# Kernel optimization log

Hardware: AMD Instinct MI355X
Metric: run time of the kernel (lower is better)

## Reference

```python
import jax, jax.numpy as jnp
import numpy as np


def _simple_rnn(x_tbd, Wx, Wh, b, return_sequences):
    # x_tbd: [T, B, D]; h_t = tanh(x_t @ Wx + h_{t-1} @ Wh + b)
    B = x_tbd.shape[1]
    H = Wh.shape[0]
    # precompute input projection for all steps (single big GEMM)
    xw = jnp.einsum('tbd,dh->tbh', x_tbd, Wx) + b

    def step(h, xw_t):
        h_new = jnp.tanh(xw_t + h @ Wh)
        return h_new, h_new if return_sequences else None

    h0 = jnp.zeros((B, H), dtype=x_tbd.dtype)
    h_last, hs = jax.lax.scan(step, h0, xw)
    return hs if return_sequences else h_last


def setup_inputs() -> dict:
    key = jax.random.key(0)
    ks = jax.random.split(key, 8)
    B, T, D, H, C = 32, 1024, 128, 512, 10
    s_in = 1.0 / np.sqrt(D)
    s_h = 1.0 / np.sqrt(H)
    return {
        'x': jax.random.normal(ks[0], (B, T, D), jnp.float32),
        'Wx1': jax.random.normal(ks[1], (D, H), jnp.float32) * s_in,
        'Wh1': jax.random.normal(ks[2], (H, H), jnp.float32) * s_h,
        'b1': jnp.zeros((H,), jnp.float32),
        'Wx2': jax.random.normal(ks[3], (H, H), jnp.float32) * s_h,
        'Wh2': jax.random.normal(ks[4], (H, H), jnp.float32) * s_h,
        'b2': jnp.zeros((H,), jnp.float32),
        'Wo': jax.random.normal(ks[5], (H, C), jnp.float32) * s_h,
        'bo': jnp.zeros((C,), jnp.float32),
    }


def reference(x, Wx1, Wh1, b1, Wx2, Wh2, b2, Wo, bo):
    # x: [B, T, D] -> time-major [T, B, D]
    x_t = jnp.swapaxes(x, 0, 1)
    h1 = _simple_rnn(x_t, Wx1, Wh1, b1, return_sequences=True)   # [T, B, H]
    h2 = _simple_rnn(h1, Wx2, Wh2, b2, return_sequences=False)   # [B, H]
    logits = h2 @ Wo + bo
    return jax.nn.softmax(logits, axis=-1)
```

## Files before the change

### kernel.cpp

```cpp
#include <hip/hip_runtime.h>
#include <hip/hip_fp16.h>
#include <math.h>

#define BATCH 32
#define TLEN  1024
#define DIN   128
#define HID   512
#define NCLS  10
#define NB    2
#define NGRP  (BATCH/NB)
#define NSL   8
#define RING  32
#define SENTV 0xFFFFFFFFu
#define SENT64 0xFFFFFFFFFFFFFFFFull
#define POLL_CAP (1u<<17)

typedef _Float16 hf2 __attribute__((ext_vector_type(2)));

__device__ __forceinline__ unsigned aload(const unsigned* p) {
  return __hip_atomic_load(p, __ATOMIC_RELAXED, __HIP_MEMORY_SCOPE_AGENT);
}
__device__ __forceinline__ void astore(unsigned* p, unsigned v) {
  __hip_atomic_store(p, v, __ATOMIC_RELAXED, __HIP_MEMORY_SCOPE_AGENT);
}
__device__ __forceinline__ unsigned long long aload64(const unsigned long long* p) {
  return __hip_atomic_load(p, __ATOMIC_RELAXED, __HIP_MEMORY_SCOPE_AGENT);
}
__device__ __forceinline__ void astore64(unsigned long long* p, unsigned long long v) {
  __hip_atomic_store(p, v, __ATOMIC_RELAXED, __HIP_MEMORY_SCOPE_AGENT);
}
__device__ __forceinline__ int aloadi(const int* p) {
  return __hip_atomic_load(p, __ATOMIC_RELAXED, __HIP_MEMORY_SCOPE_AGENT);
}
__device__ __forceinline__ void astorei(int* p, int v) {
  __hip_atomic_store(p, v, __ATOMIC_RELAXED, __HIP_MEMORY_SCOPE_AGENT);
}

__device__ __forceinline__ float fdot2u(unsigned a, unsigned b, float c) {
#if __has_builtin(__builtin_amdgcn_fdot2)
  return __builtin_amdgcn_fdot2(__builtin_bit_cast(hf2, a),
                                __builtin_bit_cast(hf2, b), c, false);
#else
  hf2 av = __builtin_bit_cast(hf2, a), bv = __builtin_bit_cast(hf2, b);
  return c + (float)av[0] * (float)bv[0] + (float)av[1] * (float)bv[1];
#endif
}

__device__ __forceinline__ unsigned packh2(float lo, float hi) {
  __half2 h = __floats2half2_rn(lo, hi);
  return __builtin_bit_cast(unsigned, h);
}

__global__ __launch_bounds__(256) void k_xw1(
    const float* __restrict__ x, const float* __restrict__ Wx1,
    const float* __restrict__ b1, unsigned* __restrict__ xw1)
{
  __shared__ float xst[DIN * 4];
  const int tid  = threadIdx.x;
  const int row0 = blockIdx.x * 4;
  for (int idx = tid; idx < 4 * DIN; idx += 256) {
    int r = idx >> 7, d = idx & (DIN - 1);
    int row = row0 + r;
    int t = row >> 5, b = row & 31;
    xst[d * 4 + r] = x[((size_t)b * TLEN + t) * DIN + d];
  }
  __syncthreads();
  float acc[4][2];
#pragma unroll
  for (int r = 0; r < 4; ++r) { acc[r][0] = 0.f; acc[r][1] = 0.f; }
  const int j0 = 2 * tid, j1 = 2 * tid + 1;
  for (int d = 0; d < DIN; ++d) {
    float w0 = Wx1[(size_t)d * HID + j0];
    float w1 = Wx1[(size_t)d * HID + j1];
    float4 xv = *reinterpret_cast<const float4*>(&xst[d * 4]);
    acc[0][0] += xv.x * w0; acc[0][1] += xv.x * w1;
    acc[1][0] += xv.y * w0; acc[1][1] += xv.y * w1;
    acc[2][0] += xv.z * w0; acc[2][1] += xv.z * w1;
    acc[3][0] += xv.w * w0; acc[3][1] += xv.w * w1;
  }
  float bb0 = b1[j0], bb1 = b1[j1];
#pragma unroll
  for (int r = 0; r < 4; ++r)
    xw1[(size_t)(row0 + r) * 256 + tid] = packh2(acc[r][0] + bb0, acc[r][1] + bb1);
}

__global__ __launch_bounds__(512) void k_rnn(
    const unsigned* __restrict__ xw1,
    const float* __restrict__ Wh1,
    const float* __restrict__ Wx2, const float* __restrict__ Wh2,
    const float* __restrict__ b2,
    unsigned* __restrict__ ring1,
    unsigned* __restrict__ ringC,
    int* __restrict__ prog2,
    float* __restrict__ h2fin)
{
  const int tid  = threadIdx.x;
  const int wgid = blockIdx.x;
  const int xcd   = wgid & 7;
  const int mm    = wgid >> 3;
  const int sl    = mm & 7;
  const int layer = (mm >> 3) & 1;
  const int g     = ((mm >> 4) << 3) | xcd;
  const int b0 = g * NB;
  const int c0 = sl * 64;
  const int w  = tid >> 6, l = tid & 63;
  const int q  = l >> 4;
  const int lo = l & 15;
  const int o  = w * 16 + lo;
  const int obb = o >> 6, oj = o & 63;
  const int ocol = c0 + oj;

  const int pu = tid & 127;

  __shared__ __align__(16) unsigned h_s[2][NB][512];

  if (layer == 0) {
    const int pb = (tid >> 7) & 1;
    unsigned wreg[64];
    {
      const int k0 = q * 128;
#pragma unroll
      for (int i = 0; i < 16; ++i) {
        const int rr = 4 * ((i + q) & 15);
#pragma unroll
        for (int j = 0; j < 4; ++j) {
          const int k = k0 + 2 * (rr + j);
          wreg[4 * i + j] = packh2(Wh1[(size_t)k * HID + ocol],
                                   Wh1[(size_t)(k + 1) * HID + ocol]);
        }
      }
    }
    int cached = -1;
    for (int t = 0; t < TLEN; ++t) {
      const int p = t & 1;
      unsigned long long v64 = 0;
      const unsigned long long* pp = nullptr;
      if (tid < 256 && t > 0) {
        pp = (const unsigned long long*)
             &ring1[((size_t)((t - 1) & (RING - 1)) * BATCH + b0 + pb) * 256 + 2 * pu];
        v64 = aload64(pp);
      }
      unsigned xww = 0;
      if (q == 0)
        xww = xw1[((size_t)t * BATCH + b0 + obb) * 256 + (ocol >> 1)];
      if (w == 0) {
        const int need = t - (RING - 6);
        if (cached < need) {
          unsigned it = 0;
          for (;;) {
            int pr = (l < NSL) ? aloadi(&prog2[g * NSL + l]) : 0x7fffffff;
#pragma unroll
            for (int d = 1; d < NSL; d <<= 1) pr = min(pr, __shfl_xor(pr, d));
            pr = __shfl(pr, 0);
            cached = pr;
            if (cached >= need || ++it >= POLL_CAP) break;
          }
        }
        if (l < 32) {
          int rb = l >> 4, jj = l & 15;
          astore64((unsigned long long*)
                   &ring1[((size_t)((t + 1) & (RING - 1)) * BATCH + b0 + rb) * 256
                          + (c0 >> 1) + 2 * jj], SENT64);
        }
      }
      if (tid < 256) {
        if (t > 0) {
          unsigned v0 = (unsigned)v64, v1 = (unsigned)(v64 >> 32);
          if (v0 == SENTV || v1 == SENTV) {
            unsigned it = 0;
            do {
              unsigned long long nv = aload64(pp);
              v0 = (unsigned)nv; v1 = (unsigned)(nv >> 32);
            } while ((v0 == SENTV || v1 == SENTV) && ++it < POLL_CAP);
            if (v0 == SENTV) v0 = 0;
            if (v1 == SENTV) v1 = 0;
            v64 = ((unsigned long long)v1 << 32) | v0;
          }
        }
        *(unsigned long long*)&h_s[p][pb][2 * pu] = v64;
      }
      __syncthreads();
      float acc = 0.f;
      const unsigned* hp = &h_s[p][obb][q * 64];
#pragma unroll
      for (int i = 0; i < 16; ++i) {
        const int rr = 4 * ((i + q) & 15);
        uint4 hv = *reinterpret_cast<const uint4*>(&hp[rr]);
        acc = fdot2u(hv.x, wreg[4 * i + 0], acc);
        acc = fdot2u(hv.y, wreg[4 * i + 1], acc);
        acc = fdot2u(hv.z, wreg[4 * i + 2], acc);
        acc = fdot2u(hv.w, wreg[4 * i + 3], acc);
      }
      acc += __shfl_xor(acc, 16);
      acc += __shfl_xor(acc, 32);
      if (q == 0) {
        hf2 xv = __builtin_bit_cast(hf2, xww);
        float z = (float)xv[oj & 1] + acc;
        float h = tanhf(z);
        float hn = __shfl_down(h, 1);
        if (!(lo & 1))
          astore(&ring1[((size_t)(t & (RING - 1)) * BATCH + b0 + obb) * 256 + (ocol >> 1)],
                 packh2(h, hn));
      }
    }
  } else {
    const int set = tid >> 7;
    unsigned wreg[128];
    {
      const int k0 = q * 256;
#pragma unroll
      for (int i = 0; i < 32; ++i) {
        const int rr = 4 * ((i + q) & 31);
#pragma unroll
        for (int j = 0; j < 4; ++j) {
          const int k = k0 + 2 * (rr + j);
          float a, b;
          if (k < HID) {
            a = Wx2[(size_t)k * HID + ocol];
            b = Wx2[(size_t)(k + 1) * HID + ocol];
          } else {
            a = Wh2[(size_t)(k - HID) * HID + ocol];
            b = Wh2[(size_t)(k - HID + 1) * HID + ocol];
          }
          wreg[4 * i + j] = packh2(a, b);
        }
      }
    }
    float b2v = (q == 0) ? b2[ocol] : 0.f;
    for (int t = 0; t < TLEN; ++t) {
      const int p = t & 1;
      unsigned long long v64 = 0;
      const unsigned long long* pp = nullptr;
      if (set < 2) {
        pp = (const unsigned long long*)
             &ring1[((size_t)(t & (RING - 1)) * BATCH + b0 + set) * 256 + 2 * pu];
        v64 = aload64(pp);
      } else if (t > 0) {
        pp = (const unsigned long long*)
             &ringC[((size_t)((t - 1) & (RING - 1)) * BATCH + b0 + (set - 2)) * 256 + 2 * pu];
        v64 = aload64(pp);
      }
      if (w == 0 && l < 32) {
        int rb = l >> 4, jj = l & 15;
        astore64((unsigned long long*)
                 &ringC[((size_t)((t + 1) & (RING - 1)) * BATCH + b0 + rb) * 256
                        + (c0 >> 1) + 2 * jj], SENT64);
      }
      if (pp) {
        unsigned v0 = (unsigned)v64, v1 = (unsigned)(v64 >> 32);
        if (v0 == SENTV || v1 == SENTV) {
          unsigned it = 0;
          do {
            unsigned long long nv = aload64(pp);
            v0 = (unsigned)nv; v1 = (unsigned)(nv >> 32);
          } while ((v0 == SENTV || v1 == SENTV) && ++it < POLL_CAP);
          if (v0 == SENTV) v0 = 0;
          if (v1 == SENTV) v1 = 0;
          v64 = ((unsigned long long)v1 << 32) | v0;
        }
      }
      {
        const int bb = set & 1;
        const int base = (set >> 1) * 256;
        *(unsigned long long*)&h_s[p][bb][base + 2 * pu] = v64;
      }
      __syncthreads();
      if (tid == 0) astorei(&prog2[g * NSL + sl], t);
      float acc = 0.f;
      const unsigned* hp = &h_s[p][obb][q * 128];
#pragma unroll
      for (int i = 0; i < 32; ++i) {
        const int rr = 4 * ((i + q) & 31);
        uint4 hv = *reinterpret_cast<const uint4*>(&hp[rr]);
        acc = fdot2u(hv.x, wreg[4 * i + 0], acc);
        acc = fdot2u(hv.y, wreg[4 * i + 1], acc);
        acc = fdot2u(hv.z, wreg[4 * i + 2], acc);
        acc = fdot2u(hv.w, wreg[4 * i + 3], acc);
      }
      acc += __shfl_xor(acc, 16);
      acc += __shfl_xor(acc, 32);
      if (q == 0) {
        float z = b2v + acc;
        float h = tanhf(z);
        if (t == TLEN - 1) h2fin[(size_t)(b0 + obb) * HID + ocol] = h;
        float hn = __shfl_down(h, 1);
        if (!(lo & 1))
          astore(&ringC[((size_t)(t & (RING - 1)) * BATCH + b0 + obb) * 256 + (ocol >> 1)],
                 packh2(h, hn));
      }
    }
  }
}

__global__ __launch_bounds__(640) void k_head(
    const float* __restrict__ h2, const float* __restrict__ Wo,
    const float* __restrict__ bo, float* __restrict__ out)
{
  __shared__ float lg[16];
  const int b = blockIdx.x;
  const int c = threadIdx.x >> 6;
  const int l = threadIdx.x & 63;
  float p = 0.f;
#pragma unroll
  for (int i = 0; i < 8; ++i) {
    int k = l + 64 * i;
    p += h2[(size_t)b * HID + k] * Wo[(size_t)k * NCLS + c];
  }
  for (int off = 32; off; off >>= 1) p += __shfl_down(p, off);
  if (l == 0) lg[c] = p + bo[c];
  __syncthreads();
  if (threadIdx.x == 0) {
    float m = lg[0];
    for (int i = 1; i < NCLS; ++i) m = fmaxf(m, lg[i]);
    float e[NCLS];
    float s = 0.f;
    for (int i = 0; i < NCLS; ++i) { e[i] = expf(lg[i] - m); s += e[i]; }
    for (int i = 0; i < NCLS; ++i) out[(size_t)b * NCLS + i] = e[i] / s;
  }
}

extern "C" void kernel_launch(void* const* d_in, const int* in_sizes, int n_in,
                              void* d_out, int out_size, void* d_ws, size_t ws_size,
                              hipStream_t stream)
{
  (void)in_sizes; (void)n_in; (void)out_size; (void)ws_size;
  const float* x   = (const float*)d_in[0];
  const float* Wx1 = (const float*)d_in[1];
  const float* Wh1 = (const float*)d_in[2];
  const float* b1  = (const float*)d_in[3];
  const float* Wx2 = (const float*)d_in[4];
  const float* Wh2 = (const float*)d_in[5];
  const float* b2  = (const float*)d_in[6];
  const float* Wo  = (const float*)d_in[7];
  const float* bo  = (const float*)d_in[8];
  float* out = (float*)d_out;

  char* ws = (char*)d_ws;
  size_t o = 0;
  unsigned* xw1 = (unsigned*)(ws + o); o += (size_t)TLEN * BATCH * 256 * 4;
  const size_t ringBytes = (size_t)RING * BATCH * 256 * 4;
  unsigned* ring1 = (unsigned*)(ws + o); o += ringBytes;
  unsigned* ringC = (unsigned*)(ws + o); o += ringBytes;
  int* prog2 = (int*)(ws + o); o += 1024;
  float* h2fin = (float*)(ws + o); o += (size_t)BATCH * HID * 4;

  hipMemsetAsync(ring1, 0xFF, 2 * ringBytes, stream);
  hipMemsetAsync(prog2, 0xFF, NGRP * NSL * 4, stream);

  k_xw1<<<TLEN * BATCH / 4, 256, 0, stream>>>(x, Wx1, b1, xw1);
  k_rnn<<<256, 512, 0, stream>>>(xw1, Wh1, Wx2, Wh2, b2,
                                 ring1, ringC, prog2, h2fin);
  k_head<<<BATCH, 640, 0, stream>>>(h2fin, Wo, bo, out);
}
```

Baseline: 1.983 ms.

## Interleave two batch pairs per workgroup to halve RNN workgroup count

Each workgroup now owns four batch rows, processed as two interleaved pairs per timestep, so the grid drops from 256 to 128 workgroups. Each pair keeps its own shared-memory buffer, progress counter and sentinel ring handshake, so while one pair waits on its ring data the workgroup can work on the other. This cuts the number of polling workgroups and the cross-XCD traffic. The cost is twice the serial per-step work in each workgroup, plus an extra __syncthreads per step. The XCD-aware workgroup mapping is also replaced by a simpler index split.

```diff
diff --git a/kernel.cpp b/kernel.cpp
--- a/kernel.cpp
+++ b/kernel.cpp
@@ -7,8 +7,7 @@
 #define DIN   128
 #define HID   512
 #define NCLS  10
-#define NB    2
-#define NGRP  (BATCH/NB)
+#define NGR   8
 #define NSL   8
 #define RING  32
 #define SENTV 0xFFFFFFFFu
@@ -96,12 +95,10 @@
 {
   const int tid  = threadIdx.x;
   const int wgid = blockIdx.x;
-  const int xcd   = wgid & 7;
-  const int mm    = wgid >> 3;
-  const int sl    = mm & 7;
-  const int layer = (mm >> 3) & 1;
-  const int g     = ((mm >> 4) << 3) | xcd;
-  const int b0 = g * NB;
+  const int g     = wgid & 7;
+  const int sl    = (wgid >> 3) & 7;
+  const int layer = wgid >> 6;
+  const int b0 = g * 4;
   const int c0 = sl * 64;
   const int w  = tid >> 6, l = tid & 63;
   const int q  = l >> 4;
@@ -112,7 +109,7 @@
 
   const int pu = tid & 127;
 
-  __shared__ __align__(16) unsigned h_s[2][NB][512];
+  __shared__ __align__(16) unsigned h_s[2][2][2][512];
 
   if (layer == 0) {
     const int pb = (tid >> 7) & 1;
@@ -130,41 +127,130 @@
         }
       }
     }
-    int cached = -1;
+    int cached[2] = {-1, -1};
     for (int t = 0; t < TLEN; ++t) {
-      const int p = t & 1;
-      unsigned long long v64 = 0;
-      const unsigned long long* pp = nullptr;
-      if (tid < 256 && t > 0) {
-        pp = (const unsigned long long*)
-             &ring1[((size_t)((t - 1) & (RING - 1)) * BATCH + b0 + pb) * 256 + 2 * pu];
-        v64 = aload64(pp);
+      const int par = t & 1;
+#pragma unroll
+      for (int pr = 0; pr < 2; ++pr) {
+        const int bbase = b0 + 2 * pr;
+        unsigned long long v64 = 0;
+        const unsigned long long* pp = nullptr;
+        if (tid < 256 && t > 0) {
+          pp = (const unsigned long long*)
+               &ring1[((size_t)((t - 1) & (RING - 1)) * BATCH + bbase + pb) * 256 + 2 * pu];
+          v64 = aload64(pp);
+        }
+        unsigned xww = 0;
+        if (q == 0)
+          xww = xw1[((size_t)t * BATCH + bbase + obb) * 256 + (ocol >> 1)];
+        if (w == 0) {
+          const int need = t - (RING - 6);
+          if (cached[pr] < need) {
+            unsigned it = 0;
+            for (;;) {
+              int p2 = (l < NSL) ? aloadi(&prog2[((g * NSL + l) << 1) + pr]) : 0x7fffffff;
+#pragma unroll
+              for (int d = 1; d < NSL; d <<= 1) p2 = min(p2, __shfl_xor(p2, d));
+              p2 = __shfl(p2, 0);
+              cached[pr] = p2;
+              if (cached[pr] >= need || ++it >= POLL_CAP) break;
+            }
+          }
+          if (l < 32) {
+            int rb = l >> 4, jj = l & 15;
+            astore64((unsigned long long*)
+                     &ring1[((size_t)((t + 1) & (RING - 1)) * BATCH + bbase + rb) * 256
+                            + (c0 >> 1) + 2 * jj], SENT64);
+          }
+        }
+        if (tid < 256) {
+          if (t > 0) {
+            unsigned v0 = (unsigned)v64, v1 = (unsigned)(v64 >> 32);
+            if (v0 == SENTV || v1 == SENTV) {
+              unsigned it = 0;
+              do {
+                unsigned long long nv = aload64(pp);
+                v0 = (unsigned)nv; v1 = (unsigned)(nv >> 32);
+              } while ((v0 == SENTV || v1 == SENTV) && ++it < POLL_CAP);
+              if (v0 == SENTV) v0 = 0;
+              if (v1 == SENTV) v1 = 0;
+              v64 = ((unsigned long long)v1 << 32) | v0;
+            }
+          }
+          *(unsigned long long*)&h_s[pr][par][pb][2 * pu] = v64;
+        }
+        __syncthreads();
+        float acc = 0.f;
+        const unsigned* hp = &h_s[pr][par][obb][q * 64];
+#pragma unroll
+        for (int i = 0; i < 16; ++i) {
+          const int rr = 4 * ((i + q) & 15);
+          uint4 hv = *reinterpret_cast<const uint4*>(&hp[rr]);
+          acc = fdot2u(hv.x, wreg[4 * i + 0], acc);
+          acc = fdot2u(hv.y, wreg[4 * i + 1], acc);
+          acc = fdot2u(hv.z, wreg[4 * i + 2], acc);
+          acc = fdot2u(hv.w, wreg[4 * i + 3], acc);
+        }
+        acc += __shfl_xor(acc, 16);
+        acc += __shfl_xor(acc, 32);
+        if (q == 0) {
+          hf2 xv = __builtin_bit_cast(hf2, xww);
+          float z = (float)xv[oj & 1] + acc;
+          float h = tanhf(z);
+          float hn = __shfl_down(h, 1);
+          if (!(lo & 1))
+            astore(&ring1[((size_t)(t & (RING - 1)) * BATCH + bbase + obb) * 256 + (ocol >> 1)],
+                   packh2(h, hn));
+        }
       }
-      unsigned xww = 0;
-      if (q == 0)
-        xww = xw1[((size_t)t * BATCH + b0 + obb) * 256 + (ocol >> 1)];
-      if (w == 0) {
-        const int need = t - (RING - 6);
-        if (cached < need) {
-          unsigned it = 0;
-          for (;;) {
-            int pr = (l < NSL) ? aloadi(&prog2[g * NSL + l]) : 0x7fffffff;
-#pragma unroll
-            for (int d = 1; d < NSL; d <<= 1) pr = min(pr, __shfl_xor(pr, d));
-            pr = __shfl(pr, 0);
-            cached = pr;
-            if (cached >= need || ++it >= POLL_CAP) break;
-          }
-        }
-        if (l < 32) {
+    }
+  } else {
+    const int set = tid >> 7;
+    unsigned wreg[128];
+    {
+      const int k0 = q * 256;
+#pragma unroll
+      for (int i = 0; i < 32; ++i) {
+        const int rr = 4 * ((i + q) & 31);
+#pragma unroll
+        for (int j = 0; j < 4; ++j) {
+          const int k = k0 + 2 * (rr + j);
+          float a, b;
+          if (k < HID) {
+            a = Wx2[(size_t)k * HID + ocol];
+            b = Wx2[(size_t)(k + 1) * HID + ocol];
+          } else {
+            a = Wh2[(size_t)(k - HID) * HID + ocol];
+            b = Wh2[(size_t)(k - HID + 1) * HID + ocol];
+          }
+          wreg[4 * i + j] = packh2(a, b);
+        }
+      }
+    }
+    float b2v = (q == 0) ? b2[ocol] : 0.f;
+    for (int t = 0; t < TLEN; ++t) {
+      const int par = t & 1;
+#pragma unroll
+      for (int pr = 0; pr < 2; ++pr) {
+        const int bbase = b0 + 2 * pr;
+        unsigned long long v64 = 0;
+        const unsigned long long* pp = nullptr;
+        if (set < 2) {
+          pp = (const unsigned long long*)
+               &ring1[((size_t)(t & (RING - 1)) * BATCH + bbase + set) * 256 + 2 * pu];
+          v64 = aload64(pp);
+        } else if (t > 0) {
+          pp = (const unsigned long long*)
+               &ringC[((size_t)((t - 1) & (RING - 1)) * BATCH + bbase + (set - 2)) * 256 + 2 * pu];
+          v64 = aload64(pp);
+        }
+        if (w == 0 && l < 32) {
           int rb = l >> 4, jj = l & 15;
           astore64((unsigned long long*)
-                   &ring1[((size_t)((t + 1) & (RING - 1)) * BATCH + b0 + rb) * 256
+                   &ringC[((size_t)((t + 1) & (RING - 1)) * BATCH + bbase + rb) * 256
                           + (c0 >> 1) + 2 * jj], SENT64);
         }
-      }
-      if (tid < 256) {
-        if (t > 0) {
+        if (pp) {
           unsigned v0 = (unsigned)v64, v1 = (unsigned)(v64 >> 32);
           if (v0 == SENTV || v1 == SENTV) {
             unsigned it = 0;
@@ -177,116 +263,35 @@
             v64 = ((unsigned long long)v1 << 32) | v0;
           }
         }
-        *(unsigned long long*)&h_s[p][pb][2 * pu] = v64;
-      }
-      __syncthreads();
-      float acc = 0.f;
-      const unsigned* hp = &h_s[p][obb][q * 64];
-#pragma unroll
-      for (int i = 0; i < 16; ++i) {
-        const int rr = 4 * ((i + q) & 15);
-        uint4 hv = *reinterpret_cast<const uint4*>(&hp[rr]);
-        acc = fdot2u(hv.x, wreg[4 * i + 0], acc);
-        acc = fdot2u(hv.y, wreg[4 * i + 1], acc);
-        acc = fdot2u(hv.z, wreg[4 * i + 2], acc);
-        acc = fdot2u(hv.w, wreg[4 * i + 3], acc);
-      }
-      acc += __shfl_xor(acc, 16);
-      acc += __shfl_xor(acc, 32);
-      if (q == 0) {
-        hf2 xv = __builtin_bit_cast(hf2, xww);
-        float z = (float)xv[oj & 1] + acc;
-        float h = tanhf(z);
-        float hn = __shfl_down(h, 1);
-        if (!(lo & 1))
-          astore(&ring1[((size_t)(t & (RING - 1)) * BATCH + b0 + obb) * 256 + (ocol >> 1)],
-                 packh2(h, hn));
-      }
-    }
-  } else {
-    const int set = tid >> 7;
-    unsigned wreg[128];
-    {
-      const int k0 = q * 256;
-#pragma unroll
-      for (int i = 0; i < 32; ++i) {
-        const int rr = 4 * ((i + q) & 31);
-#pragma unroll
-        for (int j = 0; j < 4; ++j) {
-          const int k = k0 + 2 * (rr + j);
-          float a, b;
-          if (k < HID) {
-            a = Wx2[(size_t)k * HID + ocol];
-            b = Wx2[(size_t)(k + 1) * HID + ocol];
-          } else {
-            a = Wh2[(size_t)(k - HID) * HID + ocol];
-            b = Wh2[(size_t)(k - HID + 1) * HID + ocol];
-          }
-          wreg[4 * i + j] = packh2(a, b);
-        }
-      }
-    }
-    float b2v = (q == 0) ? b2[ocol] : 0.f;
-    for (int t = 0; t < TLEN; ++t) {
-      const int p = t & 1;
-      unsigned long long v64 = 0;
-      const unsigned long long* pp = nullptr;
-      if (set < 2) {
-        pp = (const unsigned long long*)
-             &ring1[((size_t)(t & (RING - 1)) * BATCH + b0 + set) * 256 + 2 * pu];
-        v64 = aload64(pp);
-      } else if (t > 0) {
-        pp = (const unsigned long long*)
-             &ringC[((size_t)((t - 1) & (RING - 1)) * BATCH + b0 + (set - 2)) * 256 + 2 * pu];
-        v64 = aload64(pp);
-      }
-      if (w == 0 && l < 32) {
-        int rb = l >> 4, jj = l & 15;
-        astore64((unsigned long long*)
-                 &ringC[((size_t)((t + 1) & (RING - 1)) * BATCH + b0 + rb) * 256
-                        + (c0 >> 1) + 2 * jj], SENT64);
-      }
-      if (pp) {
-        unsigned v0 = (unsigned)v64, v1 = (unsigned)(v64 >> 32);
-        if (v0 == SENTV || v1 == SENTV) {
-          unsigned it = 0;
-          do {
-            unsigned long long nv = aload64(pp);
-            v0 = (unsigned)nv; v1 = (unsigned)(nv >> 32);
-          } while ((v0 == SENTV || v1 == SENTV) && ++it < POLL_CAP);
-          if (v0 == SENTV) v0 = 0;
-          if (v1 == SENTV) v1 = 0;
-          v64 = ((unsigned long long)v1 << 32) | v0;
-        }
-      }
-      {
-        const int bb = set & 1;
-        const int base = (set >> 1) * 256;
-        *(unsigned long long*)&h_s[p][bb][base + 2 * pu] = v64;
-      }
-      __syncthreads();
-      if (tid == 0) astorei(&prog2[g * NSL + sl], t);
-      float acc = 0.f;
-      const unsigned* hp = &h_s[p][obb][q * 128];
-#pragma unroll
-      for (int i = 0; i < 32; ++i) {
-        const int rr = 4 * ((i + q) & 31);
-        uint4 hv = *reinterpret_cast<const uint4*>(&hp[rr]);
-        acc = fdot2u(hv.x, wreg[4 * i + 0], acc);
-        acc = fdot2u(hv.y, wreg[4 * i + 1], acc);
-        acc = fdot2u(hv.z, wreg[4 * i + 2], acc);
-        acc = fdot2u(hv.w, wreg[4 * i + 3], acc);
-      }
-      acc += __shfl_xor(acc, 16);
-      acc += __shfl_xor(acc, 32);
-      if (q == 0) {
-        float z = b2v + acc;
-        float h = tanhf(z);
-        if (t == TLEN - 1) h2fin[(size_t)(b0 + obb) * HID + ocol] = h;
-        float hn = __shfl_down(h, 1);
-        if (!(lo & 1))
-          astore(&ringC[((size_t)(t & (RING - 1)) * BATCH + b0 + obb) * 256 + (ocol >> 1)],
-                 packh2(h, hn));
+        {
+          const int bb = set & 1;
+          const int base = (set >> 1) * 256;
+          *(unsigned long long*)&h_s[pr][par][bb][base + 2 * pu] = v64;
+        }
+        __syncthreads();
+        if (tid == 0) astorei(&prog2[((g * NSL + sl) << 1) + pr], t);
+        float acc = 0.f;
+        const unsigned* hp = &h_s[pr][par][obb][q * 128];
+#pragma unroll
+        for (int i = 0; i < 32; ++i) {
+          const int rr = 4 * ((i + q) & 31);
+          uint4 hv = *reinterpret_cast<const uint4*>(&hp[rr]);
+          acc = fdot2u(hv.x, wreg[4 * i + 0], acc);
+          acc = fdot2u(hv.y, wreg[4 * i + 1], acc);
+          acc = fdot2u(hv.z, wreg[4 * i + 2], acc);
+          acc = fdot2u(hv.w, wreg[4 * i + 3], acc);
+        }
+        acc += __shfl_xor(acc, 16);
+        acc += __shfl_xor(acc, 32);
+        if (q == 0) {
+          float z = b2v + acc;
+          float h = tanhf(z);
+          if (t == TLEN - 1) h2fin[(size_t)(bbase + obb) * HID + ocol] = h;
+          float hn = __shfl_down(h, 1);
+          if (!(lo & 1))
+            astore(&ringC[((size_t)(t & (RING - 1)) * BATCH + bbase + obb) * 256 + (ocol >> 1)],
+                   packh2(h, hn));
+        }
       }
     }
   }
@@ -345,10 +350,10 @@
   float* h2fin = (float*)(ws + o); o += (size_t)BATCH * HID * 4;
 
   hipMemsetAsync(ring1, 0xFF, 2 * ringBytes, stream);
-  hipMemsetAsync(prog2, 0xFF, NGRP * NSL * 4, stream);
+  hipMemsetAsync(prog2, 0xFF, 1024, stream);
 
   k_xw1<<<TLEN * BATCH / 4, 256, 0, stream>>>(x, Wx1, b1, xw1);
-  k_rnn<<<256, 512, 0, stream>>>(xw1, Wh1, Wx2, Wh2, b2,
-                                 ring1, ringC, prog2, h2fin);
+  k_rnn<<<NGR * NSL * 2, 512, 0, stream>>>(xw1, Wh1, Wx2, Wh2, b2,
+                                           ring1, ringC, prog2, h2fin);
   k_head<<<BATCH, 640, 0, stream>>>(h2fin, Wo, bo, out);
 }
```

After: 2.788 ms. 1.41x slower.

## Add duplicate fast-path ring buffers with sc0 cache-coherent loads for inter-block handoff

Applied to the files above, without the earlier changes.

Each ring (ring1/ringC) gets a twin buffer that is written and polled with inline-asm global loads and stores using the sc0 cache bit, instead of agent-scope atomics. Consumers poll the fast copy first and fall back to the atomic copy every fourth iteration. Producers now pack 64-bit stores, four halves per lane, through an extra shuffle. The aim is lower latency for the per-timestep cross-workgroup handoff. The cost is doubled ring traffic and reliance on sc0 coherence between XCDs, which may return stale data; the atomic fallback exists to cover that.

```diff
diff --git a/kernel.cpp b/kernel.cpp
--- a/kernel.cpp
+++ b/kernel.cpp
@@ -17,12 +17,6 @@
 
 typedef _Float16 hf2 __attribute__((ext_vector_type(2)));
 
-__device__ __forceinline__ unsigned aload(const unsigned* p) {
-  return __hip_atomic_load(p, __ATOMIC_RELAXED, __HIP_MEMORY_SCOPE_AGENT);
-}
-__device__ __forceinline__ void astore(unsigned* p, unsigned v) {
-  __hip_atomic_store(p, v, __ATOMIC_RELAXED, __HIP_MEMORY_SCOPE_AGENT);
-}
 __device__ __forceinline__ unsigned long long aload64(const unsigned long long* p) {
   return __hip_atomic_load(p, __ATOMIC_RELAXED, __HIP_MEMORY_SCOPE_AGENT);
 }
@@ -34,6 +28,17 @@
 }
 __device__ __forceinline__ void astorei(int* p, int v) {
   __hip_atomic_store(p, v, __ATOMIC_RELAXED, __HIP_MEMORY_SCOPE_AGENT);
+}
+
+__device__ __forceinline__ unsigned long long fload(const unsigned long long* p) {
+  unsigned long long r;
+  asm volatile("global_load_dwordx2 %0, %1, off sc0\n\ts_waitcnt vmcnt(0)"
+               : "=v"(r) : "v"(p) : "memory");
+  return r;
+}
+__device__ __forceinline__ void fstore(unsigned long long* p, unsigned long long v) {
+  asm volatile("global_store_dwordx2 %0, %1, off sc0"
+               :: "v"(p), "v"(v) : "memory");
 }
 
 __device__ __forceinline__ float fdot2u(unsigned a, unsigned b, float c) {
@@ -49,6 +54,29 @@
 __device__ __forceinline__ unsigned packh2(float lo, float hi) {
   __half2 h = __floats2half2_rn(lo, hi);
   return __builtin_bit_cast(unsigned, h);
+}
+
+__device__ __forceinline__ unsigned long long resolve64(
+    unsigned long long v64, const unsigned long long* pf,
+    const unsigned long long* ps)
+{
+  unsigned v0 = (unsigned)v64, v1 = (unsigned)(v64 >> 32);
+  if (v0 == SENTV || v1 == SENTV) {
+    unsigned it = 0;
+    for (;;) {
+      unsigned long long nv = fload(pf);
+      v0 = (unsigned)nv; v1 = (unsigned)(nv >> 32);
+      if ((v0 != SENTV && v1 != SENTV) || it >= POLL_CAP) break;
+      if ((++it & 3) == 3) {
+        nv = aload64(ps);
+        v0 = (unsigned)nv; v1 = (unsigned)(nv >> 32);
+        if (v0 != SENTV && v1 != SENTV) break;
+      }
+    }
+    if (v0 == SENTV) v0 = 0;
+    if (v1 == SENTV) v1 = 0;
+  }
+  return ((unsigned long long)v1 << 32) | v0;
 }
 
 __global__ __launch_bounds__(256) void k_xw1(
@@ -89,8 +117,10 @@
     const float* __restrict__ Wh1,
     const float* __restrict__ Wx2, const float* __restrict__ Wh2,
     const float* __restrict__ b2,
-    unsigned* __restrict__ ring1,
-    unsigned* __restrict__ ringC,
+    unsigned long long* __restrict__ ring1,
+    unsigned long long* __restrict__ ringC,
+    unsigned long long* __restrict__ fast1,
+    unsigned long long* __restrict__ fastC,
     int* __restrict__ prog2,
     float* __restrict__ h2fin)
 {
@@ -134,11 +164,11 @@
     for (int t = 0; t < TLEN; ++t) {
       const int p = t & 1;
       unsigned long long v64 = 0;
-      const unsigned long long* pp = nullptr;
+      const unsigned long long *pf = nullptr, *ps = nullptr;
       if (tid < 256 && t > 0) {
-        pp = (const unsigned long long*)
-             &ring1[((size_t)((t - 1) & (RING - 1)) * BATCH + b0 + pb) * 256 + 2 * pu];
-        v64 = aload64(pp);
+        const size_t off = ((size_t)((t - 1) & (RING - 1)) * BATCH + b0 + pb) * 128 + pu;
+        pf = &fast1[off]; ps = &ring1[off];
+        v64 = fload(pf);
       }
       unsigned xww = 0;
       if (q == 0)
@@ -156,27 +186,16 @@
             if (cached >= need || ++it >= POLL_CAP) break;
           }
         }
-        if (l < 32) {
-          int rb = l >> 4, jj = l & 15;
-          astore64((unsigned long long*)
-                   &ring1[((size_t)((t + 1) & (RING - 1)) * BATCH + b0 + rb) * 256
-                          + (c0 >> 1) + 2 * jj], SENT64);
+        {
+          const int hl = l & 31;
+          const size_t off = ((size_t)((t + 1) & (RING - 1)) * BATCH + b0 + (hl >> 4)) * 128
+                             + (c0 >> 2) + (hl & 15);
+          if (l < 32) astore64(&ring1[off], SENT64);
+          else        fstore(&fast1[off], SENT64);
         }
       }
       if (tid < 256) {
-        if (t > 0) {
-          unsigned v0 = (unsigned)v64, v1 = (unsigned)(v64 >> 32);
-          if (v0 == SENTV || v1 == SENTV) {
-            unsigned it = 0;
-            do {
-              unsigned long long nv = aload64(pp);
-              v0 = (unsigned)nv; v1 = (unsigned)(nv >> 32);
-            } while ((v0 == SENTV || v1 == SENTV) && ++it < POLL_CAP);
-            if (v0 == SENTV) v0 = 0;
-            if (v1 == SENTV) v1 = 0;
-            v64 = ((unsigned long long)v1 << 32) | v0;
-          }
-        }
+        if (t > 0) v64 = resolve64(v64, pf, ps);
         *(unsigned long long*)&h_s[p][pb][2 * pu] = v64;
       }
       __syncthreads();
@@ -198,9 +217,15 @@
         float z = (float)xv[oj & 1] + acc;
         float h = tanhf(z);
         float hn = __shfl_down(h, 1);
-        if (!(lo & 1))
-          astore(&ring1[((size_t)(t & (RING - 1)) * BATCH + b0 + obb) * 256 + (ocol >> 1)],
-                 packh2(h, hn));
+        unsigned u = packh2(h, hn);
+        unsigned u2 = __shfl_down(u, 2);
+        if (!(lo & 3)) {
+          unsigned long long uv = ((unsigned long long)u2 << 32) | u;
+          const size_t off = ((size_t)(t & (RING - 1)) * BATCH + b0 + obb) * 128
+                             + ((c0 + oj) >> 2);
+          fstore(&fast1[off], uv);
+          astore64(&ring1[off], uv);
+        }
       }
     }
   } else {
@@ -230,35 +255,24 @@
     for (int t = 0; t < TLEN; ++t) {
       const int p = t & 1;
       unsigned long long v64 = 0;
-      const unsigned long long* pp = nullptr;
+      const unsigned long long *pf = nullptr, *ps = nullptr;
       if (set < 2) {
-        pp = (const unsigned long long*)
-             &ring1[((size_t)(t & (RING - 1)) * BATCH + b0 + set) * 256 + 2 * pu];
-        v64 = aload64(pp);
+        const size_t off = ((size_t)(t & (RING - 1)) * BATCH + b0 + set) * 128 + pu;
+        pf = &fast1[off]; ps = &ring1[off];
+        v64 = fload(pf);
       } else if (t > 0) {
-        pp = (const unsigned long long*)
-             &ringC[((size_t)((t - 1) & (RING - 1)) * BATCH + b0 + (set - 2)) * 256 + 2 * pu];
-        v64 = aload64(pp);
-      }
-      if (w == 0 && l < 32) {
-        int rb = l >> 4, jj = l & 15;
-        astore64((unsigned long long*)
-                 &ringC[((size_t)((t + 1) & (RING - 1)) * BATCH + b0 + rb) * 256
-                        + (c0 >> 1) + 2 * jj], SENT64);
-      }
-      if (pp) {
-        unsigned v0 = (unsigned)v64, v1 = (unsigned)(v64 >> 32);
-        if (v0 == SENTV || v1 == SENTV) {
-          unsigned it = 0;
-          do {
-            unsigned long long nv = aload64(pp);
-            v0 = (unsigned)nv; v1 = (unsigned)(nv >> 32);
-          } while ((v0 == SENTV || v1 == SENTV) && ++it < POLL_CAP);
-          if (v0 == SENTV) v0 = 0;
-          if (v1 == SENTV) v1 = 0;
-          v64 = ((unsigned long long)v1 << 32) | v0;
-        }
-      }
+        const size_t off = ((size_t)((t - 1) & (RING - 1)) * BATCH + b0 + (set - 2)) * 128 + pu;
+        pf = &fastC[off]; ps = &ringC[off];
+        v64 = fload(pf);
+      }
+      if (w == 0) {
+        const int hl = l & 31;
+        const size_t off = ((size_t)((t + 1) & (RING - 1)) * BATCH + b0 + (hl >> 4)) * 128
+                           + (c0 >> 2) + (hl & 15);
+        if (l < 32) astore64(&ringC[off], SENT64);
+        else        fstore(&fastC[off], SENT64);
+      }
+      if (pf) v64 = resolve64(v64, pf, ps);
       {
         const int bb = set & 1;
         const int base = (set >> 1) * 256;
@@ -284,9 +298,15 @@
         float h = tanhf(z);
         if (t == TLEN - 1) h2fin[(size_t)(b0 + obb) * HID + ocol] = h;
         float hn = __shfl_down(h, 1);
-        if (!(lo & 1))
-          astore(&ringC[((size_t)(t & (RING - 1)) * BATCH + b0 + obb) * 256 + (ocol >> 1)],
-                 packh2(h, hn));
+        unsigned u = packh2(h, hn);
+        unsigned u2 = __shfl_down(u, 2);
+        if (!(lo & 3)) {
+          unsigned long long uv = ((unsigned long long)u2 << 32) | u;
+          const size_t off = ((size_t)(t & (RING - 1)) * BATCH + b0 + obb) * 128
+                             + ((c0 + oj) >> 2);
+          fstore(&fastC[off], uv);
+          astore64(&ringC[off], uv);
+        }
       }
     }
   }
@@ -338,17 +358,19 @@
   char* ws = (char*)d_ws;
   size_t o = 0;
   unsigned* xw1 = (unsigned*)(ws + o); o += (size_t)TLEN * BATCH * 256 * 4;
-  const size_t ringBytes = (size_t)RING * BATCH * 256 * 4;
-  unsigned* ring1 = (unsigned*)(ws + o); o += ringBytes;
-  unsigned* ringC = (unsigned*)(ws + o); o += ringBytes;
+  const size_t ringBytes = (size_t)RING * BATCH * 128 * 8;
+  unsigned long long* ring1 = (unsigned long long*)(ws + o); o += ringBytes;
+  unsigned long long* ringC = (unsigned long long*)(ws + o); o += ringBytes;
+  unsigned long long* fast1 = (unsigned long long*)(ws + o); o += ringBytes;
+  unsigned long long* fastC = (unsigned long long*)(ws + o); o += ringBytes;
   int* prog2 = (int*)(ws + o); o += 1024;
   float* h2fin = (float*)(ws + o); o += (size_t)BATCH * HID * 4;
 
-  hipMemsetAsync(ring1, 0xFF, 2 * ringBytes, stream);
+  hipMemsetAsync(ring1, 0xFF, 4 * ringBytes, stream);
   hipMemsetAsync(prog2, 0xFF, NGRP * NSL * 4, stream);
 
   k_xw1<<<TLEN * BATCH / 4, 256, 0, stream>>>(x, Wx1, b1, xw1);
   k_rnn<<<256, 512, 0, stream>>>(xw1, Wh1, Wx2, Wh2, b2,
-                                 ring1, ringC, prog2, h2fin);
+                                 ring1, ringC, fast1, fastC, prog2, h2fin);
   k_head<<<BATCH, 640, 0, stream>>>(h2fin, Wo, bo, out);
 }
```

Result: slower. 2.167 ms (+9.3%).
